# Performance work log

Measured on AMD Instinct MI355X. Metric: run time of the kernel, lower is better.

## Reference

```python
import jax, jax.numpy as jnp
import numpy as np

T, N, F, H, C, E = 8, 50000, 128, 64, 4, 800000


def setup_inputs() -> dict:
    key = jax.random.key(0)
    ks = jax.random.split(key, 8)
    x = jax.random.normal(ks[0], (T, N, F), jnp.float32)
    edges = jax.random.randint(ks[1], (T, 2, E), 0, N, jnp.int32)
    # GCNConv weights (one per timestep, glorot-ish scale) + Linear layers
    Wg = jax.random.normal(ks[2], (T, F, H), jnp.float32) / np.sqrt(F)
    bg = jnp.zeros((T, H), jnp.float32)
    W1 = jax.random.normal(ks[3], (H, 32), jnp.float32) / np.sqrt(H)
    b1 = jnp.zeros((32,), jnp.float32)
    W2 = jax.random.normal(ks[4], (32, 16), jnp.float32) / np.sqrt(32)
    b2 = jnp.zeros((16,), jnp.float32)
    W3 = jax.random.normal(ks[5], (16, C), jnp.float32) / np.sqrt(16)
    b3 = jnp.zeros((C,), jnp.float32)
    return dict(x=x, edges=edges, Wg=Wg, bg=bg, W1=W1, b1=b1, W2=W2, b2=b2, W3=W3, b3=b3)


def gcn_conv(x, edge_index, W, b):
    """PyG GCNConv: add self-loops, sym-normalized aggregation of x @ W, plus bias."""
    n = x.shape[0]
    loop = jnp.arange(n, dtype=edge_index.dtype)
    src = jnp.concatenate([edge_index[0], loop])  # message sources
    dst = jnp.concatenate([edge_index[1], loop])  # aggregation targets
    deg = jax.ops.segment_sum(jnp.ones_like(dst, dtype=x.dtype), dst, num_segments=n)
    dinv = jnp.where(deg > 0, jax.lax.rsqrt(deg), 0.0)
    xw = x @ W                                    # [n, H]
    norm = (dinv[src] * dinv[dst])[:, None]       # [E+n, 1]
    out = jax.ops.segment_sum(xw[src] * norm, dst, num_segments=n)
    return out + b


def reference(x, edges, Wg, bg, W1, b1, W2, b2, W3, b3):
    def step(acc, inp):
        xt, et, Wt, bt = inp
        return acc + jax.nn.relu(gcn_conv(xt, et, Wt, bt)), None

    acc0 = jnp.zeros((x.shape[1], Wg.shape[-1]), x.dtype)
    h, _ = jax.lax.scan(step, acc0, (x, edges, Wg, bg))  # sum over T timesteps
    h = jax.nn.relu(h)                 # dropout omitted (eval mode)
    h = jax.nn.relu(h @ W1 + b1)
    h = jax.nn.relu(h @ W2 + b2)
    logits = h @ W3 + b3
    return jax.nn.log_softmax(logits, axis=1)
```

## Files before the change

kernel.cpp:

```cpp
#include <hip/hip_runtime.h>
#include <hip/hip_bf16.h>

#define TT 8
#define NN 50000
#define FF 128
#define HH 64
#define CC 4
#define EE 800000
#define NB2 391
#define CAP 2560
#define BPT 128

typedef unsigned short u16;
typedef unsigned int u32;
typedef __attribute__((ext_vector_type(8))) short bf16x8;
typedef __attribute__((ext_vector_type(4))) float f32x4;

static __device__ __forceinline__ float bflo(u32 w) {
    union { unsigned int i; float f; } v; v.i = w << 16; return v.f;
}
static __device__ __forceinline__ float bfhi(u32 w) {
    union { unsigned int i; float f; } v; v.i = w & 0xFFFF0000u; return v.f;
}
static __device__ __forceinline__ u16 cvt_bf16(float f) {
    __hip_bfloat16 b = __float2bfloat16(f);
    return *reinterpret_cast<u16*>(&b);
}

__global__ __launch_bounds__(256) void zero_gcur_kernel(int* __restrict__ gcur) {
    int i = blockIdx.x * 256 + threadIdx.x;
    if (i < TT * NB2) gcur[i] = 0;
}

__global__ __launch_bounds__(256) void multisplit_kernel(const int* __restrict__ edges,
                                                         int* __restrict__ gcur, u32* __restrict__ binned) {
    __shared__ u32 sbuf[NB2][16];
    __shared__ int scnt[NB2];
    int bid = blockIdx.x;
    int t = bid & 7;
    int blk = bid >> 3;
    const int per = (EE + BPT - 1) / BPT;
    int e0 = blk * per;
    int e1 = e0 + per; if (e1 > EE) e1 = EE;

    for (int i = threadIdx.x; i < NB2; i += 256) scnt[i] = 0;
    __syncthreads();

    const int* es = edges + (size_t)(t * 2 + 0) * EE;
    const int* ed = edges + (size_t)(t * 2 + 1) * EE;
    int* gc = gcur + t * NB2;
    u32* bb = binned + (size_t)t * NB2 * CAP;

    for (int base = e0; base < e1; base += 512) {
        u32 recA = 0, recB = 0; int bA = -1, bB = -1;
        int eA = base + threadIdx.x;
        int eB = base + 256 + threadIdx.x;
        if (eA < e1) {
            int src = es[eA], dst = ed[eA];
            bA = dst >> 7;
            recA = (u32)src | ((u32)(dst & 127) << 16);
            int p = atomicAdd(&scnt[bA], 1);
            if (p < 16) { sbuf[bA][p] = recA; bA = -1; }
        }
        if (eB < e1) {
            int src = es[eB], dst = ed[eB];
            bB = dst >> 7;
            recB = (u32)src | ((u32)(dst & 127) << 16);
            int p = atomicAdd(&scnt[bB], 1);
            if (p < 16) { sbuf[bB][p] = recB; bB = -1; }
        }
        __syncthreads();
        for (int fb = threadIdx.x; fb < NB2; fb += 256) {
            if (scnt[fb] >= 16) {
                int g = atomicAdd(&gc[fb], 16);
                uint4* dp = (uint4*)(bb + (size_t)fb * CAP + g);
                uint4* sp = (uint4*)&sbuf[fb][0];
                dp[0] = sp[0]; dp[1] = sp[1]; dp[2] = sp[2]; dp[3] = sp[3];
                scnt[fb] = 0;
            }
        }
        __syncthreads();
        if (bA >= 0) {
            int p = atomicAdd(&scnt[bA], 1);
            if (p < 16) sbuf[bA][p] = recA;
            else { int g = atomicAdd(&gc[bA], 1); bb[(size_t)bA * CAP + g] = recA; }
        }
        if (bB >= 0) {
            int p = atomicAdd(&scnt[bB], 1);
            if (p < 16) sbuf[bB][p] = recB;
            else { int g = atomicAdd(&gc[bB], 1); bb[(size_t)bB * CAP + g] = recB; }
        }
        __syncthreads();
    }
    for (int fb = threadIdx.x; fb < NB2; fb += 256) {
        int c = scnt[fb];
        if (c > 0) {
            int g = atomicAdd(&gc[fb], c);
            for (int k = 0; k < c; ++k) bb[(size_t)fb * CAP + g + k] = sbuf[fb][k];
        }
    }
}

__global__ __launch_bounds__(256) void csr_scatter_kernel(const u32* __restrict__ binned, const int* __restrict__ gcur,
                                                          u16* __restrict__ srclist, u32* __restrict__ nodeinfo,
                                                          float* __restrict__ dinv) {
    __shared__ u32 recs[CAP];
    __shared__ int hist[128];
    __shared__ int cur[128];
    int b = blockIdx.x, t = blockIdx.y, tid = threadIdx.x;
    int node0 = b * 128;
    int tot = gcur[t * NB2 + b];
    const u32* win = binned + ((size_t)t * NB2 + b) * CAP;

    for (int i = tid; i < tot; i += 256) recs[i] = win[i];
    if (tid < 128) hist[tid] = 0;
    __syncthreads();
    for (int i = tid; i < tot; i += 256) atomicAdd(&hist[recs[i] >> 16], 1);
    __syncthreads();
    if (tid < 64) {
        int v0 = hist[2 * tid], v1 = hist[2 * tid + 1];
        int pair = v0 + v1;
        int inc = pair;
        #pragma unroll
        for (int off = 1; off < 64; off <<= 1) {
            int u = __shfl_up(inc, off, 64);
            if (tid >= off) inc += u;
        }
        int exclp = inc - pair;
        cur[2 * tid] = exclp;
        cur[2 * tid + 1] = exclp + v0;
        int node = node0 + 2 * tid;
        if (node < NN) {
            nodeinfo[t * NN + node] = (u32)(b * CAP + exclp) | ((u32)v0 << 20);
            dinv[t * NN + node] = rsqrtf(1.0f + (float)v0);
        }
        if (node + 1 < NN) {
            nodeinfo[t * NN + node + 1] = (u32)(b * CAP + exclp + v0) | ((u32)v1 << 20);
            dinv[t * NN + node + 1] = rsqrtf(1.0f + (float)v1);
        }
    }
    __syncthreads();
    u16* sl = srclist + (size_t)t * NB2 * CAP;
    for (int i = tid; i < tot; i += 256) {
        u32 rec = recs[i];
        int d = rec >> 16;
        int p = atomicAdd(&cur[d], 1);
        sl[(size_t)b * CAP + p] = (u16)(rec & 0xFFFF);
    }
}

__global__ __launch_bounds__(256) void wt_prep_kernel(const float* __restrict__ Wg, u16* __restrict__ wt) {
    int t = blockIdx.x;
    const float* w = Wg + t * FF * HH;
    u16* o = wt + (size_t)t * HH * FF;
    for (int i = threadIdx.x; i < FF * HH; i += 256) {
        int k = i >> 6, c = i & 63;
        o[c * FF + k] = cvt_bf16(w[i]);
    }
}

__global__ __launch_bounds__(512) void xw_kernel(const float* __restrict__ x, const u16* __restrict__ wt,
                                                 const float* __restrict__ dinv, u16* __restrict__ y) {
    int t = blockIdx.y;
    int row0 = blockIdx.x * 256;
    int tid = threadIdx.x;
    int w = tid >> 6, lane = tid & 63;
    int l15 = lane & 15, lg = lane >> 4;
    __shared__ __align__(16) u16 ylds[256][72];
    const float* xt = x + (size_t)t * NN * FF;
    const u16* wtt = wt + (size_t)t * HH * FF;

    f32x4 d[2][4] = {{{0,0,0,0},{0,0,0,0},{0,0,0,0},{0,0,0,0}},
                     {{0,0,0,0},{0,0,0,0},{0,0,0,0},{0,0,0,0}}};
    #pragma unroll
    for (int k0 = 0; k0 < 128; k0 += 32) {
        int kb = k0 + lg * 8;
        union { bf16x8 v; __hip_bfloat162 h[4]; } au[2];
        #pragma unroll
        for (int s = 0; s < 2; ++s) {
            int arow = row0 + w * 32 + s * 16 + l15;
            if (arow < NN) {
                float4 f0 = *reinterpret_cast<const float4*>(&xt[(size_t)arow * FF + kb]);
                float4 f1 = *reinterpret_cast<const float4*>(&xt[(size_t)arow * FF + kb + 4]);
                au[s].h[0] = __float22bfloat162_rn(make_float2(f0.x, f0.y));
                au[s].h[1] = __float22bfloat162_rn(make_float2(f0.z, f0.w));
                au[s].h[2] = __float22bfloat162_rn(make_float2(f1.x, f1.y));
                au[s].h[3] = __float22bfloat162_rn(make_float2(f1.z, f1.w));
            } else {
                au[s].v = (bf16x8){0,0,0,0,0,0,0,0};
            }
        }
        #pragma unroll
        for (int n = 0; n < 4; ++n) {
            bf16x8 bf = *reinterpret_cast<const bf16x8*>(&wtt[(size_t)(n * 16 + l15) * FF + kb]);
            d[0][n] = __builtin_amdgcn_mfma_f32_16x16x32_bf16(au[0].v, bf, d[0][n], 0, 0, 0);
            d[1][n] = __builtin_amdgcn_mfma_f32_16x16x32_bf16(au[1].v, bf, d[1][n], 0, 0, 0);
        }
    }
    #pragma unroll
    for (int s = 0; s < 2; ++s) {
        int rl = w * 32 + s * 16 + lg * 4;
        float dv[4];
        #pragma unroll
        for (int i = 0; i < 4; ++i) {
            int grow = row0 + rl + i;
            dv[i] = (grow < NN) ? dinv[t * NN + grow] : 0.f;
        }
        #pragma unroll
        for (int n = 0; n < 4; ++n) {
            int col = n * 16 + l15;
            #pragma unroll
            for (int i = 0; i < 4; ++i)
                ylds[rl + i][col] = cvt_bf16(d[s][n][i] * dv[i]);
        }
    }
    __syncthreads();
    u16* yt = y + (size_t)t * NN * HH;
    #pragma unroll
    for (int it = 0; it < 4; ++it) {
        int idx = it * 512 + tid;
        int r = idx >> 3, c8 = (idx & 7) * 8;
        int grow = row0 + r;
        if (grow < NN)
            *reinterpret_cast<uint4*>(&yt[(size_t)grow * HH + c8]) =
                *reinterpret_cast<const uint4*>(&ylds[r][c8]);
    }
}

__global__ __launch_bounds__(256) void agg_kernel(const u16* __restrict__ y, const float* __restrict__ dinv,
                                                  const u32* __restrict__ nodeinfo, const u16* __restrict__ srclist,
                                                  const float* __restrict__ bg, float* __restrict__ acc) {
    int node = blockIdx.x * 4 + (threadIdx.x >> 6);
    int lane = threadIdx.x & 63;
    int sub = lane >> 4;
    int fo = lane & 15;
    float a0 = 0.f, a1 = 0.f, a2 = 0.f, a3 = 0.f;
    for (int t = 0; t < TT; ++t) {
        const u16* yt = y + (size_t)t * NN * HH;
        u32 info = nodeinfo[t * NN + node];
        int cnt = info >> 20;
        const u16* sl = srclist + (size_t)t * NB2 * CAP + (info & 0xFFFFF);
        float s0 = 0.f, s1 = 0.f, s2 = 0.f, s3 = 0.f;
        int j = 0;
        for (; j + 16 <= cnt; j += 16) {
            int e0 = sl[j + sub], e1 = sl[j + 4 + sub], e2 = sl[j + 8 + sub], e3 = sl[j + 12 + sub];
            uint2 v0 = *reinterpret_cast<const uint2*>(&yt[(size_t)e0 * HH + fo * 4]);
            uint2 v1 = *reinterpret_cast<const uint2*>(&yt[(size_t)e1 * HH + fo * 4]);
            uint2 v2 = *reinterpret_cast<const uint2*>(&yt[(size_t)e2 * HH + fo * 4]);
            uint2 v3 = *reinterpret_cast<const uint2*>(&yt[(size_t)e3 * HH + fo * 4]);
            s0 += (bflo(v0.x) + bflo(v1.x)) + (bflo(v2.x) + bflo(v3.x));
            s1 += (bfhi(v0.x) + bfhi(v1.x)) + (bfhi(v2.x) + bfhi(v3.x));
            s2 += (bflo(v0.y) + bflo(v1.y)) + (bflo(v2.y) + bflo(v3.y));
            s3 += (bfhi(v0.y) + bfhi(v1.y)) + (bfhi(v2.y) + bfhi(v3.y));
        }
        for (; j < cnt; j += 4) {
            int e = j + sub;
            uint2 v = make_uint2(0u, 0u);
            if (e < cnt) {
                int srcid = sl[e];
                v = *reinterpret_cast<const uint2*>(&yt[(size_t)srcid * HH + fo * 4]);
            }
            s0 += bflo(v.x);
            s1 += bfhi(v.x);
            s2 += bflo(v.y);
            s3 += bfhi(v.y);
        }
        s0 += __shfl_xor(s0, 16, 64); s0 += __shfl_xor(s0, 32, 64);
        s1 += __shfl_xor(s1, 16, 64); s1 += __shfl_xor(s1, 32, 64);
        s2 += __shfl_xor(s2, 16, 64); s2 += __shfl_xor(s2, 32, 64);
        s3 += __shfl_xor(s3, 16, 64); s3 += __shfl_xor(s3, 32, 64);
        uint2 sv = *reinterpret_cast<const uint2*>(&yt[(size_t)node * HH + fo * 4]);
        s0 += bflo(sv.x);
        s1 += bfhi(sv.x);
        s2 += bflo(sv.y);
        s3 += bfhi(sv.y);
        float dvv = dinv[t * NN + node];
        float4 bgv = *reinterpret_cast<const float4*>(&bg[t * HH + fo * 4]);
        a0 += fmaxf(dvv * s0 + bgv.x, 0.f);
        a1 += fmaxf(dvv * s1 + bgv.y, 0.f);
        a2 += fmaxf(dvv * s2 + bgv.z, 0.f);
        a3 += fmaxf(dvv * s3 + bgv.w, 0.f);
    }
    if (sub == 0) {
        float4 o = make_float4(a0, a1, a2, a3);
        *reinterpret_cast<float4*>(&acc[(size_t)node * HH + fo * 4]) = o;
    }
}

__global__ __launch_bounds__(256) void head_kernel(const float* __restrict__ acc,
                                                   const float* __restrict__ W1, const float* __restrict__ b1,
                                                   const float* __restrict__ W2, const float* __restrict__ b2,
                                                   const float* __restrict__ W3, const float* __restrict__ b3,
                                                   float* __restrict__ out) {
    __shared__ float w1[64 * 32], w2[32 * 16], w3[16 * 4], bb1[32], bb2[16], bb3[4];
    int tid = threadIdx.x;
    for (int i = tid; i < 2048; i += 256) w1[i] = W1[i];
    for (int i = tid; i < 512; i += 256) w2[i] = W2[i];
    if (tid < 64) w3[tid] = W3[tid];
    if (tid < 32) bb1[tid] = b1[tid];
    if (tid < 16) bb2[tid] = b2[tid];
    if (tid < 4) bb3[tid] = b3[tid];
    __syncthreads();
    int node = blockIdx.x * 256 + tid;
    if (node >= NN) return;

    float a[64];
    #pragma unroll
    for (int k = 0; k < 64; ++k) a[k] = acc[(size_t)node * HH + k];

    float h1[32];
    for (int j = 0; j < 32; ++j) {
        float s = bb1[j];
        #pragma unroll
        for (int k = 0; k < 64; ++k) s += a[k] * w1[k * 32 + j];
        h1[j] = fmaxf(s, 0.f);
    }
    float h2[16];
    for (int j = 0; j < 16; ++j) {
        float s = bb2[j];
        #pragma unroll
        for (int k = 0; k < 32; ++k) s += h1[k] * w2[k * 16 + j];
        h2[j] = fmaxf(s, 0.f);
    }
    float l[4];
    for (int c = 0; c < 4; ++c) {
        float s = bb3[c];
        #pragma unroll
        for (int k = 0; k < 16; ++k) s += h2[k] * w3[k * 4 + c];
        l[c] = s;
    }
    float m = fmaxf(fmaxf(l[0], l[1]), fmaxf(l[2], l[3]));
    float sum = 0.f;
    #pragma unroll
    for (int c = 0; c < 4; ++c) sum += expf(l[c] - m);
    float lse = logf(sum);
    float4 o;
    o.x = l[0] - m - lse; o.y = l[1] - m - lse; o.z = l[2] - m - lse; o.w = l[3] - m - lse;
    *reinterpret_cast<float4*>(&out[(size_t)node * CC]) = o;
}

extern "C" void kernel_launch(void* const* d_in, const int* in_sizes, int n_in,
                              void* d_out, int out_size, void* d_ws, size_t ws_size,
                              hipStream_t stream) {
    const float* x    = (const float*)d_in[0];
    const int*  edges = (const int*)d_in[1];
    const float* Wg   = (const float*)d_in[2];
    const float* bg   = (const float*)d_in[3];
    const float* W1   = (const float*)d_in[4];
    const float* b1   = (const float*)d_in[5];
    const float* W2   = (const float*)d_in[6];
    const float* b2   = (const float*)d_in[7];
    const float* W3   = (const float*)d_in[8];
    const float* b3   = (const float*)d_in[9];
    float* out = (float*)d_out;

    char* ws = (char*)d_ws;
    size_t o = 0;
    int* gcur      = (int*)(ws + o); o += (size_t)TT * NB2 * 4;
    o = (o + 255) & ~(size_t)255;
    float* dinv    = (float*)(ws + o); o += (size_t)TT * NN * 4;
    u32* nodeinfo  = (u32*)(ws + o); o += (size_t)TT * NN * 4;
    o = (o + 255) & ~(size_t)255;
    u16* wt        = (u16*)(ws + o); o += (size_t)TT * HH * FF * 2;
    o = (o + 255) & ~(size_t)255;
    u32* binned    = (u32*)(ws + o); o += (size_t)TT * NB2 * CAP * 4;
    u16* srclist   = (u16*)(ws + o); o += (size_t)TT * NB2 * CAP * 2;
    u16* y         = (u16*)(ws + o); o += (size_t)TT * NN * HH * 2;
    float* acc     = (float*)(ws + o); o += (size_t)NN * HH * 4;

    zero_gcur_kernel<<<(TT * NB2 + 255) / 256, 256, 0, stream>>>(gcur);

    multisplit_kernel<<<BPT * TT, 256, 0, stream>>>(edges, gcur, binned);

    dim3 gsc(NB2, TT);
    csr_scatter_kernel<<<gsc, 256, 0, stream>>>(binned, gcur, srclist, nodeinfo, dinv);

    wt_prep_kernel<<<TT, 256, 0, stream>>>(Wg, wt);

    dim3 gx(196, TT);
    xw_kernel<<<gx, 512, 0, stream>>>(x, wt, dinv, y);

    agg_kernel<<<12500, 256, 0, stream>>>(y, dinv, nodeinfo, srclist, bg, acc);

    head_kernel<<<196, 256, 0, stream>>>(acc, W1, b1, W2, b2, W3, b3, out);
}
```

Measured before the change: 350.6 us.

## Vectorize edge loads in multisplit, widen CSR scatter, nontemporal x loads

The multisplit kernel now has each thread load four edges at once with 128-bit loads, processing 1024 edges per iteration. BPT changes to 125 so EE divides evenly and the bounds clamp can go. The CSR scatter kernel moves from 256 to 512 threads per block, and the x loads in xw_kernel become nontemporal loads so the single-use stream does not pollute cache. These are several separate bandwidth and latency tweaks spread across three kernels, and the four pending records per thread raise register pressure in the multisplit loop.

After: 338.3 us. -3.5%, faster.

```diff
diff --git a/kernel.cpp b/kernel.cpp
--- a/kernel.cpp
+++ b/kernel.cpp
@@ -9,12 +9,13 @@
 #define EE 800000
 #define NB2 391
 #define CAP 2560
-#define BPT 128
+#define BPT 125
 
 typedef unsigned short u16;
 typedef unsigned int u32;
 typedef __attribute__((ext_vector_type(8))) short bf16x8;
 typedef __attribute__((ext_vector_type(4))) float f32x4;
+typedef __attribute__((ext_vector_type(4))) int i32x4;
 
 static __device__ __forceinline__ float bflo(u32 w) {
     union { unsigned int i; float f; } v; v.i = w << 16; return v.f;
@@ -39,9 +40,9 @@
     int bid = blockIdx.x;
     int t = bid & 7;
     int blk = bid >> 3;
-    const int per = (EE + BPT - 1) / BPT;
+    const int per = EE / BPT;
     int e0 = blk * per;
-    int e1 = e0 + per; if (e1 > EE) e1 = EE;
+    int e1 = e0 + per;
 
     for (int i = threadIdx.x; i < NB2; i += 256) scnt[i] = 0;
     __syncthreads();
@@ -51,23 +52,36 @@
     int* gc = gcur + t * NB2;
     u32* bb = binned + (size_t)t * NB2 * CAP;
 
-    for (int base = e0; base < e1; base += 512) {
-        u32 recA = 0, recB = 0; int bA = -1, bB = -1;
-        int eA = base + threadIdx.x;
-        int eB = base + 256 + threadIdx.x;
-        if (eA < e1) {
-            int src = es[eA], dst = ed[eA];
-            bA = dst >> 7;
-            recA = (u32)src | ((u32)(dst & 127) << 16);
-            int p = atomicAdd(&scnt[bA], 1);
-            if (p < 16) { sbuf[bA][p] = recA; bA = -1; }
-        }
-        if (eB < e1) {
-            int src = es[eB], dst = ed[eB];
-            bB = dst >> 7;
-            recB = (u32)src | ((u32)(dst & 127) << 16);
-            int p = atomicAdd(&scnt[bB], 1);
-            if (p < 16) { sbuf[bB][p] = recB; bB = -1; }
+    for (int base = e0; base < e1; base += 1024) {
+        u32 rec[4]; int pb[4];
+        int e = base + threadIdx.x * 4;
+        int nv = 0;
+        if (e + 3 < e1) nv = 4;
+        else if (e < e1) nv = e1 - e;
+        if (nv == 4) {
+            i32x4 s4 = *reinterpret_cast<const i32x4*>(&es[e]);
+            i32x4 d4 = *reinterpret_cast<const i32x4*>(&ed[e]);
+            #pragma unroll
+            for (int q = 0; q < 4; ++q) {
+                int b = d4[q] >> 7;
+                u32 r = (u32)s4[q] | ((u32)(d4[q] & 127) << 16);
+                int p = atomicAdd(&scnt[b], 1);
+                if (p < 16) { sbuf[b][p] = r; pb[q] = -1; }
+                else { rec[q] = r; pb[q] = b; }
+            }
+        } else {
+            #pragma unroll
+            for (int q = 0; q < 4; ++q) {
+                pb[q] = -1;
+                if (q < nv) {
+                    int src = es[e + q], dst = ed[e + q];
+                    int b = dst >> 7;
+                    u32 r = (u32)src | ((u32)(dst & 127) << 16);
+                    int p = atomicAdd(&scnt[b], 1);
+                    if (p < 16) sbuf[b][p] = r;
+                    else { rec[q] = r; pb[q] = b; }
+                }
+            }
         }
         __syncthreads();
         for (int fb = threadIdx.x; fb < NB2; fb += 256) {
@@ -80,15 +94,13 @@
             }
         }
         __syncthreads();
-        if (bA >= 0) {
-            int p = atomicAdd(&scnt[bA], 1);
-            if (p < 16) sbuf[bA][p] = recA;
-            else { int g = atomicAdd(&gc[bA], 1); bb[(size_t)bA * CAP + g] = recA; }
-        }
-        if (bB >= 0) {
-            int p = atomicAdd(&scnt[bB], 1);
-            if (p < 16) sbuf[bB][p] = recB;
-            else { int g = atomicAdd(&gc[bB], 1); bb[(size_t)bB * CAP + g] = recB; }
+        #pragma unroll
+        for (int q = 0; q < 4; ++q) {
+            if (pb[q] >= 0) {
+                int p = atomicAdd(&scnt[pb[q]], 1);
+                if (p < 16) sbuf[pb[q]][p] = rec[q];
+                else { int g = atomicAdd(&gc[pb[q]], 1); bb[(size_t)pb[q] * CAP + g] = rec[q]; }
+            }
         }
         __syncthreads();
     }
@@ -101,7 +113,7 @@
     }
 }
 
-__global__ __launch_bounds__(256) void csr_scatter_kernel(const u32* __restrict__ binned, const int* __restrict__ gcur,
+__global__ __launch_bounds__(512) void csr_scatter_kernel(const u32* __restrict__ binned, const int* __restrict__ gcur,
                                                           u16* __restrict__ srclist, u32* __restrict__ nodeinfo,
                                                           float* __restrict__ dinv) {
     __shared__ u32 recs[CAP];
@@ -112,10 +124,10 @@
     int tot = gcur[t * NB2 + b];
     const u32* win = binned + ((size_t)t * NB2 + b) * CAP;
 
-    for (int i = tid; i < tot; i += 256) recs[i] = win[i];
+    for (int i = tid; i < tot; i += 512) recs[i] = win[i];
     if (tid < 128) hist[tid] = 0;
     __syncthreads();
-    for (int i = tid; i < tot; i += 256) atomicAdd(&hist[recs[i] >> 16], 1);
+    for (int i = tid; i < tot; i += 512) atomicAdd(&hist[recs[i] >> 16], 1);
     __syncthreads();
     if (tid < 64) {
         int v0 = hist[2 * tid], v1 = hist[2 * tid + 1];
@@ -141,7 +153,7 @@
     }
     __syncthreads();
     u16* sl = srclist + (size_t)t * NB2 * CAP;
-    for (int i = tid; i < tot; i += 256) {
+    for (int i = tid; i < tot; i += 512) {
         u32 rec = recs[i];
         int d = rec >> 16;
         int p = atomicAdd(&cur[d], 1);
@@ -180,12 +192,12 @@
         for (int s = 0; s < 2; ++s) {
             int arow = row0 + w * 32 + s * 16 + l15;
             if (arow < NN) {
-                float4 f0 = *reinterpret_cast<const float4*>(&xt[(size_t)arow * FF + kb]);
-                float4 f1 = *reinterpret_cast<const float4*>(&xt[(size_t)arow * FF + kb + 4]);
-                au[s].h[0] = __float22bfloat162_rn(make_float2(f0.x, f0.y));
-                au[s].h[1] = __float22bfloat162_rn(make_float2(f0.z, f0.w));
-                au[s].h[2] = __float22bfloat162_rn(make_float2(f1.x, f1.y));
-                au[s].h[3] = __float22bfloat162_rn(make_float2(f1.z, f1.w));
+                f32x4 f0 = __builtin_nontemporal_load(reinterpret_cast<const f32x4*>(&xt[(size_t)arow * FF + kb]));
+                f32x4 f1 = __builtin_nontemporal_load(reinterpret_cast<const f32x4*>(&xt[(size_t)arow * FF + kb + 4]));
+                au[s].h[0] = __float22bfloat162_rn(make_float2(f0[0], f0[1]));
+                au[s].h[1] = __float22bfloat162_rn(make_float2(f0[2], f0[3]));
+                au[s].h[2] = __float22bfloat162_rn(make_float2(f1[0], f1[1]));
+                au[s].h[3] = __float22bfloat162_rn(make_float2(f1[2], f1[3]));
             } else {
                 au[s].v = (bf16x8){0,0,0,0,0,0,0,0};
             }
@@ -373,7 +385,7 @@
     multisplit_kernel<<<BPT * TT, 256, 0, stream>>>(edges, gcur, binned);
 
     dim3 gsc(NB2, TT);
-    csr_scatter_kernel<<<gsc, 256, 0, stream>>>(binned, gcur, srclist, nodeinfo, dinv);
+    csr_scatter_kernel<<<gsc, 512, 0, stream>>>(binned, gcur, srclist, nodeinfo, dinv);
 
     wt_prep_kernel<<<TT, 256, 0, stream>>>(Wg, wt);
 
```
